# Kernel tuning notes

Measured on AMD Instinct MI355X. Metric: run time of the kernel, lower is better.

## Reference

```python
import jax, jax.numpy as jnp
import numpy as np
import math

B, T = 32, 64
VOCAB = 50005
EMB = 512
HID = 1024
SES = 1024
KNOW = 8785
NEG = math.exp(-100)

def _glorot(key, shape):
    fan_in, fan_out = shape[1], shape[0]
    lim = (6.0 / (fan_in + fan_out)) ** 0.5
    return jax.random.uniform(key, shape, jnp.float32, -lim, lim)

def setup_inputs() -> dict:
    key = jax.random.key(0)
    ks = jax.random.split(key, 16)
    inp = {}
    inp['ses_encoding'] = jax.random.normal(ks[0], (B, 1, SES), jnp.float32)
    inp['know_encoding'] = jax.random.normal(ks[1], (B, 1, SES), jnp.float32)
    inp['target'] = jax.random.randint(ks[2], (B, T), 0, 50000)
    inp['embed_w'] = jax.random.normal(ks[3], (VOCAB, EMB), jnp.float32) * 0.02
    # GRU params (PyTorch layout: W_ih [3H, E], W_hh [3H, H], gate order r,z,n)
    s = 1.0 / (HID ** 0.5)
    inp['W_ih'] = jax.random.uniform(ks[4], (3 * HID, EMB), jnp.float32, -s, s)
    inp['W_hh'] = jax.random.uniform(ks[5], (3 * HID, HID), jnp.float32, -s, s)
    inp['b_ih'] = jax.random.uniform(ks[6], (3 * HID,), jnp.float32, -s, s)
    inp['b_hh'] = jax.random.uniform(ks[7], (3 * HID,), jnp.float32, -s, s)
    inp['ses_to_dec_w'] = _glorot(ks[8], (HID, SES))
    inp['ses_to_dec_b'] = jnp.zeros((HID,), jnp.float32)
    inp['dec_inf_w'] = _glorot(ks[9], (2 * EMB, HID))
    inp['ses_inf_w'] = _glorot(ks[10], (2 * EMB, SES))
    inp['emb_inf_w'] = _glorot(ks[11], (2 * EMB, EMB))
    inp['emb_inf_b'] = jnp.zeros((2 * EMB,), jnp.float32)
    inp['W1'] = jax.random.normal(ks[12], (VOCAB, SES), jnp.float32) * 0.02
    inp['W2'] = jax.random.normal(ks[13], (VOCAB, SES), jnp.float32) * 0.02
    inp['W3'] = jax.random.normal(ks[14], (VOCAB, 2 * EMB), jnp.float32) * 0.02
    inp['W4'] = jax.random.normal(ks[15], (VOCAB, EMB), jnp.float32) * 0.02
    inp['know_vote_w'] = _glorot(jax.random.fold_in(key, 99), (KNOW, SES))
    return inp

def _gru_step(x, h, W_ih, W_hh, b_ih, b_hh):
    # x: [B,E], h: [B,H]
    gi = x @ W_ih.T + b_ih
    gh = h @ W_hh.T + b_hh
    ir, iz, inn = jnp.split(gi, 3, axis=-1)
    hr, hz, hn = jnp.split(gh, 3, axis=-1)
    r = jax.nn.sigmoid(ir + hr)
    z = jax.nn.sigmoid(iz + hz)
    n = jnp.tanh(inn + r * hn)
    return (1.0 - z) * h + z * n  # torch: h' = (1-z)*n + z*h with torch z; note torch formula

def _gru_step_torch(x, h, W_ih, W_hh, b_ih, b_hh):
    gi = x @ W_ih.T + b_ih
    gh = h @ W_hh.T + b_hh
    ir, iz, inn = jnp.split(gi, 3, axis=-1)
    hr, hz, hn = jnp.split(gh, 3, axis=-1)
    r = jax.nn.sigmoid(ir + hr)
    z = jax.nn.sigmoid(iz + hz)
    n = jnp.tanh(inn + r * hn)
    return (1.0 - z) * n + z * h

def reference(ses_encoding, know_encoding, target, embed_w, W_ih, W_hh, b_ih, b_hh,
              ses_to_dec_w, ses_to_dec_b, dec_inf_w, ses_inf_w, emb_inf_w, emb_inf_b,
              W1, W2, W3, W4, know_vote_w):
    ses = ses_encoding[:, 0, :]    # [B, SES]
    know = know_encoding[:, 0, :]  # [B, SES]
    target_emb = embed_w[target]   # [B, T, E]

    h0 = jnp.tanh(ses @ ses_to_dec_w.T + ses_to_dec_b)  # [B, H]

    # time-invariant pieces
    ses_inf_vec = ses @ ses_inf_w.T                      # [B, 2E]
    l1 = ses @ W1.T                                      # [B, V]
    l2 = know @ W2.T                                     # [B, V]
    # knowledge mixture log-probs (constant over time)
    ks = know @ know_vote_w.T                            # [B, KNOW]
    ks = ks[:, :-1]                                      # drop last -> [B, KNOW-1]
    pad_l = jnp.full((ks.shape[0], 10), NEG, ks.dtype)
    pad_r = jnp.full((ks.shape[0], VOCAB - 10 - (KNOW - 1)), NEG, ks.dtype)
    know_scores = jnp.concatenate([pad_l, ks, pad_r], axis=1)  # [B, V]
    know_probs = jax.nn.log_softmax(know_scores, axis=-1)      # [B, V]
    gate_const = l1 + l2                                 # [B, V]

    def step(h, emb_t):
        # emb_t: [B, E]
        h_new = _gru_step_torch(emb_t, h, W_ih, W_hh, b_ih, b_hh)  # [B, H]
        dec_hid_vec = h_new @ dec_inf_w.T                          # [B, 2E]
        target_inf = emb_t @ emb_inf_w.T + emb_inf_b               # [B, 2E]
        total = dec_hid_vec + ses_inf_vec + target_inf             # [B, 2E]
        mx = jnp.max(total.reshape(total.shape[0], EMB, 2), axis=-1)  # maxout -> [B, E]
        logits = mx @ embed_w.T                                    # shared embedding -> [B, V]
        hid_probs = jax.nn.log_softmax(logits, axis=-1)
        l3 = h_new @ W3.T                                          # note: W3 applied to hid_o [B,H]... but W3 is [V,2E]
        l4 = emb_t @ W4.T                                          # [B, V]
        gate = jax.nn.sigmoid(gate_const + l3 + l4)                # [B, V]
        final = gate * hid_probs + (1.0 - gate) * know_probs       # [B, V]
        return h_new, final

    # target_emb time-major for scan
    _, outs = jax.lax.scan(step, h0, jnp.swapaxes(target_emb, 0, 1))
    final_scores_all = jnp.swapaxes(outs, 0, 1)  # [B, T, V]
    return final_scores_all
```

## Files before the change

### kernel.cpp

```cpp
#include <hip/hip_runtime.h>

constexpr int VOC  = 50005;
constexpr int VOCP = 50048;
constexpr int VOCP2= 50176;
constexpr int NTM  = 391;
constexpr int NTMP = 400;
constexpr int KSN  = 8784;
constexpr int KSNP = 8832;
constexpr float NPAD = 41221.0f;

typedef unsigned short u16;
typedef __attribute__((ext_vector_type(4))) float f32x4;
typedef __attribute__((ext_vector_type(8))) short bf16x8;

__device__ __forceinline__ float dot4(float4 a, float4 b) {
    return a.x*b.x + a.y*b.y + a.z*b.z + a.w*b.w;
}
__device__ __forceinline__ float sigmoidf_(float x) { return 1.0f / (1.0f + expf(-x)); }
__device__ __forceinline__ u16 f2bf(float f) {
    unsigned x = __float_as_uint(f);
    return (u16)((x + 0x7FFFu + ((x >> 16) & 1u)) >> 16);
}
__device__ __forceinline__ float bf2f(u16 u) { return __uint_as_float(((unsigned)u) << 16); }
template<int AUX>
__device__ __forceinline__ void gload_lds16x(const void* g, void* l) {
    __builtin_amdgcn_global_load_lds((const __attribute__((address_space(1))) unsigned int*)g,
                                     (__attribute__((address_space(3))) unsigned int*)l, 16, 0, AUX);
}
__device__ __forceinline__ void gload_lds16(const void* g, void* l) { gload_lds16x<0>(g, l); }
__device__ __forceinline__ void store_u16_sc(u16* p, u16 v) {
    asm volatile("global_store_short %0, %1, off sc0 sc1" :: "v"(p), "v"((unsigned)v) : "memory");
}

__global__ __launch_bounds__(256) void k_cvt(const float* __restrict__ src, u16* __restrict__ dst,
                                             int ncols, int sld, int dld) {
    int row = blockIdx.x;
    int c = (blockIdx.y * 256 + threadIdx.x) * 4;
    if (c >= ncols) return;
    float4 v = *(const float4*)(src + (size_t)row * sld + c);
    unsigned lo = f2bf(v.x) | ((unsigned)f2bf(v.y) << 16);
    unsigned hi = f2bf(v.z) | ((unsigned)f2bf(v.w) << 16);
    *(uint2*)(dst + (size_t)row * dld + c) = make_uint2(lo, hi);
}

__global__ __launch_bounds__(256) void k_pad0(u16* __restrict__ Aemb, u16* __restrict__ A34,
                                              u16* __restrict__ Awk) {
    int r = VOC + blockIdx.x;
    unsigned* p3 = (unsigned*)(A34 + (size_t)r * 1536);
    for (int i = threadIdx.x; i < 768; i += 256) p3[i] = 0;
    if (r < VOCP) {
        unsigned* pe = (unsigned*)(Aemb + (size_t)r * 512);
        if (threadIdx.x < 256) pe[threadIdx.x] = 0;
        unsigned* pw = (unsigned*)(Awk + (size_t)r * 2048);
        for (int i = threadIdx.x; i < 1024; i += 256) pw[i] = 0;
    }
}
__global__ __launch_bounds__(256) void k_padK(u16* __restrict__ kvwb) {
    int r = KSN + blockIdx.x;
    unsigned* p = (unsigned*)(kvwb + (size_t)r * 1024);
    for (int i = threadIdx.x; i < 512; i += 256) p[i] = 0;
}

__global__ __launch_bounds__(256) void k_bsk(const float* __restrict__ ses,
                                             const float* __restrict__ know,
                                             u16* __restrict__ Bsk) {
    int row = blockIdx.x;
    for (int c0 = threadIdx.x * 4; c0 < 2048; c0 += 1024) {
        uint2 val = make_uint2(0, 0);
        if (row < 32) {
            const float* srcp = (c0 < 1024) ? ses + (size_t)row * 1024 + c0
                                            : know + (size_t)row * 1024 + (c0 - 1024);
            float4 v = *(const float4*)srcp;
            val = make_uint2(f2bf(v.x) | ((unsigned)f2bf(v.y) << 16),
                             f2bf(v.z) | ((unsigned)f2bf(v.w) << 16));
        }
        *(uint2*)(Bsk + (size_t)row * 2048 + c0) = val;
    }
}

__global__ __launch_bounds__(128) void k_gather(const float* __restrict__ embed,
                                                const int* __restrict__ target,
                                                u16* __restrict__ BG) {
    int n = blockIdx.x;
    int row = target[n];
    int c = threadIdx.x * 4;
    float4 v = *(const float4*)(embed + (size_t)row * 512 + c);
    unsigned lo = f2bf(v.x) | ((unsigned)f2bf(v.y) << 16);
    unsigned hi = f2bf(v.z) | ((unsigned)f2bf(v.w) << 16);
    *(uint2*)(BG + (size_t)n * 1536 + 1024 + c) = make_uint2(lo, hi);
}

__global__ __launch_bounds__(256) void k_h0_sesinf(const float* __restrict__ ses,
                                                   const float* __restrict__ sdw,
                                                   const float* __restrict__ sdb,
                                                   const float* __restrict__ siw,
                                                   float* __restrict__ h0,
                                                   float* __restrict__ sesinf) {
    int g = blockIdx.x * 256 + threadIdx.x;
    int b = g & 31;
    int jg = g >> 5;
    int j0 = jg * 4;
    const float4* s4 = (const float4*)(ses + (size_t)b * 1024);
    const float4* wa[4];
    const float4* wc[4];
#pragma unroll
    for (int r = 0; r < 4; ++r) {
        wa[r] = (const float4*)(sdw + (size_t)(j0 + r) * 1024);
        wc[r] = (const float4*)(siw + (size_t)(j0 + r) * 1024);
    }
    float a[4] = {0, 0, 0, 0}, c[4] = {0, 0, 0, 0};
    for (int kq = 0; kq < 256; ++kq) {
        float4 sv = s4[kq];
#pragma unroll
        for (int r = 0; r < 4; ++r) { a[r] += dot4(sv, wa[r][kq]); c[r] += dot4(sv, wc[r][kq]); }
    }
#pragma unroll
    for (int r = 0; r < 4; ++r) {
        h0[b * 1024 + j0 + r] = tanhf(a[r] + sdb[j0 + r]);
        sesinf[b * 1024 + j0 + r] = c[r];
    }
}

__global__ __launch_bounds__(256) void k_lseknow(const float* __restrict__ ks,
                                                 float* __restrict__ lsek) {
    int b = blockIdx.x;
    int t = threadIdx.x;
    __shared__ float sm[256];
    float m = -1e30f;
    for (int j = t; j < KSN; j += 256) m = fmaxf(m, ks[(size_t)b * KSN + j]);
    sm[t] = m;
    __syncthreads();
    for (int s = 128; s > 0; s >>= 1) { if (t < s) sm[t] = fmaxf(sm[t], sm[t + s]); __syncthreads(); }
    m = fmaxf(sm[0], 0.0f);
    __syncthreads();
    float s = 0.0f;
    for (int j = t; j < KSN; j += 256) s += expf(ks[(size_t)b * KSN + j] - m);
    sm[t] = s;
    __syncthreads();
    for (int r = 128; r > 0; r >>= 1) { if (t < r) sm[t] += sm[t + r]; __syncthreads(); }
    if (t == 0) lsek[b] = m + logf(sm[0] + NPAD * expf(0.0f - m));
}

template<int EPI>
__global__ __launch_bounds__(256) void gemm_bt(
    const u16* __restrict__ A, int lda,
    const u16* __restrict__ B, int ldb, int K,
    const float* __restrict__ p0, const float* __restrict__ p1,
    float* __restrict__ q0, u16* __restrict__ q1,
    unsigned char* __restrict__ q2, float* __restrict__ q3)
{
    __shared__ u16 Asm[128 * 64];
    __shared__ u16 Bsm[128 * 64];
    const int tid = threadIdx.x;
    const int lane = tid & 63;
    const int w = tid >> 6;
    const int wm = w >> 1, wn = w & 1;
    const int nt = blockIdx.x, mt = blockIdx.y;

    f32x4 acc[4][4];
#pragma unroll
    for (int i = 0; i < 4; ++i)
#pragma unroll
        for (int j = 0; j < 4; ++j) acc[i][j] = (f32x4){0.f, 0.f, 0.f, 0.f};

    for (int kt = 0; kt < K; kt += 64) {
#pragma unroll
        for (int p = 0; p < 4; ++p) {
            int flat = (w * 4 + p) * 64 + lane;
            int row = flat >> 3, slot = flat & 7;
            int ss = slot ^ (row & 7);
            gload_lds16(A + (size_t)(mt * 128 + row) * lda + kt + ss * 8, Asm + flat * 8);
            gload_lds16(B + (size_t)(nt * 128 + row) * ldb + kt + ss * 8, Bsm + flat * 8);
        }
        __syncthreads();
#pragma unroll
        for (int kc = 0; kc < 2; ++kc) {
            bf16x8 af[4], bfr[4];
#pragma unroll
            for (int mi = 0; mi < 4; ++mi) {
                int row = wm * 64 + mi * 16 + (lane & 15);
                int bcol = kc * 64 + ((lane >> 4) << 4);
                af[mi] = *(const bf16x8*)((const char*)Asm + row * 128 + (bcol ^ ((row & 7) << 4)));
            }
#pragma unroll
            for (int ni = 0; ni < 4; ++ni) {
                int row = wn * 64 + ni * 16 + (lane & 15);
                int bcol = kc * 64 + ((lane >> 4) << 4);
                bfr[ni] = *(const bf16x8*)((const char*)Bsm + row * 128 + (bcol ^ ((row & 7) << 4)));
            }
#pragma unroll
            for (int mi = 0; mi < 4; ++mi)
#pragma unroll
                for (int ni = 0; ni < 4; ++ni)
                    acc[mi][ni] = __builtin_amdgcn_mfma_f32_16x16x32_bf16(af[mi], bfr[ni], acc[mi][ni], 0, 0, 0);
        }
        __syncthreads();
    }

    const int cl = lane & 15;
    const int rg = (lane >> 4) << 2;

    if constexpr (EPI == 0) {
#pragma unroll
        for (int mi = 0; mi < 4; ++mi) {
            int m0 = mt * 128 + wm * 64 + mi * 16 + rg;
            float4 bias = *(const float4*)(p0 + m0);
#pragma unroll
            for (int ni = 0; ni < 4; ++ni) {
                int n = nt * 128 + wn * 64 + ni * 16 + cl;
                float4 v;
                v.x = acc[mi][ni][0] + bias.x; v.y = acc[mi][ni][1] + bias.y;
                v.z = acc[mi][ni][2] + bias.z; v.w = acc[mi][ni][3] + bias.w;
                *(float4*)(q0 + (size_t)n * 3072 + m0) = v;
            }
        }
    }
    if constexpr (EPI == 1) {
#pragma unroll
        for (int mi = 0; mi < 4; ++mi) {
            int m0 = mt * 128 + wm * 64 + mi * 16 + rg;
            float4 eb4 = *(const float4*)(p1 + m0);
#pragma unroll
            for (int ni = 0; ni < 4; ++ni) {
                int n = nt * 128 + wn * 64 + ni * 16 + cl;
                int b = n >> 6;
                float v0 = acc[mi][ni][0] + p0[b * 1024 + m0 + 0] + eb4.x;
                float v1 = acc[mi][ni][1] + p0[b * 1024 + m0 + 1] + eb4.y;
                float v2 = acc[mi][ni][2] + p0[b * 1024 + m0 + 2] + eb4.z;
                float v3 = acc[mi][ni][3] + p0[b * 1024 + m0 + 3] + eb4.w;
                unsigned pk = f2bf(fmaxf(v0, v1)) | ((unsigned)f2bf(fmaxf(v2, v3)) << 16);
                *(unsigned*)(q1 + (size_t)n * 512 + (m0 >> 1)) = pk;
            }
        }
    }
    if constexpr (EPI == 3) {
        __shared__ float redm[2][128];
        __shared__ float reds[2][128];
#pragma unroll
        for (int mi = 0; mi < 4; ++mi) {
            int v0 = mt * 128 + wm * 64 + mi * 16 + rg;
#pragma unroll
            for (int ni = 0; ni < 4; ++ni) {
                int n = nt * 128 + wn * 64 + ni * 16 + cl;
                unsigned lo = f2bf(acc[mi][ni][0]) | ((unsigned)f2bf(acc[mi][ni][1]) << 16);
                unsigned hi = f2bf(acc[mi][ni][2]) | ((unsigned)f2bf(acc[mi][ni][3]) << 16);
                *(uint2*)(q1 + (size_t)n * VOCP + v0) = make_uint2(lo, hi);
            }
        }
#pragma unroll
        for (int ni = 0; ni < 4; ++ni) {
            float lm = -1e30f;
#pragma unroll
            for (int mi = 0; mi < 4; ++mi) {
                int v0 = mt * 128 + wm * 64 + mi * 16 + rg;
#pragma unroll
                for (int r = 0; r < 4; ++r)
                    if (v0 + r < VOC) lm = fmaxf(lm, acc[mi][ni][r]);
            }
            lm = fmaxf(lm, __shfl_xor(lm, 16));
            lm = fmaxf(lm, __shfl_xor(lm, 32));
            float s = 0.0f;
#pragma unroll
            for (int mi = 0; mi < 4; ++mi) {
                int v0 = mt * 128 + wm * 64 + mi * 16 + rg;
#pragma unroll
                for (int r = 0; r < 4; ++r)
                    if (v0 + r < VOC) s += expf(acc[mi][ni][r] - lm);
            }
            s += __shfl_xor(s, 16);
            s += __shfl_xor(s, 32);
            if (lane < 16) {
                redm[wm][wn * 64 + ni * 16 + lane] = lm;
                reds[wm][wn * 64 + ni * 16 + lane] = s;
            }
        }
        __syncthreads();
        if (tid < 128) {
            float m0_ = redm[0][tid], m1_ = redm[1][tid];
            float m = fmaxf(m0_, m1_);
            float s = reds[0][tid] * expf(m0_ - m) + reds[1][tid] * expf(m1_ - m);
            int n = nt * 128 + tid;
            q0[(size_t)n * NTMP + mt] = m;
            q3[(size_t)n * NTMP + mt] = s;
        }
    }
    if constexpr (EPI == 4) {
#pragma unroll
        for (int mi = 0; mi < 4; ++mi) {
            int m0 = mt * 128 + wm * 64 + mi * 16 + rg;
#pragma unroll
            for (int ni = 0; ni < 4; ++ni) {
                int n = nt * 128 + wn * 64 + ni * 16 + cl;
                if (n < 32) {
                    float4 v;
                    v.x = acc[mi][ni][0]; v.y = acc[mi][ni][1];
                    v.z = acc[mi][ni][2]; v.w = acc[mi][ni][3];
                    *(float4*)(q0 + (size_t)n * VOCP2 + m0) = v;
                }
            }
        }
    }
    if constexpr (EPI == 5) {
#pragma unroll
        for (int mi = 0; mi < 4; ++mi) {
            int m0 = mt * 128 + wm * 64 + mi * 16 + rg;
#pragma unroll
            for (int ni = 0; ni < 4; ++ni) {
                int n = nt * 128 + wn * 64 + ni * 16 + cl;
                if (n < 32 && m0 < KSN) {
                    float4 v;
                    v.x = acc[mi][ni][0]; v.y = acc[mi][ni][1];
                    v.z = acc[mi][ni][2]; v.w = acc[mi][ni][3];
                    *(float4*)(q0 + (size_t)n * KSN + m0) = v;
                }
            }
        }
    }
}

__global__ __launch_bounds__(512, 2) void gemm_gate8(
    const u16* __restrict__ A,
    const u16* __restrict__ B,
    const float* __restrict__ gc2,
    unsigned char* __restrict__ g8)
{
    constexpr int K = 1536, NT = K / 32;
    __shared__ __align__(16) char smem[98304];
    const int tid = threadIdx.x;
    const int lane = tid & 63;
    const int w = tid >> 6;
    const int wm = w >> 2;
    const int wn = w & 3;
    const int lrow = lane & 15;
    const int g = lane >> 4;

    int bid = blockIdx.x;
    int wg = (bid & 7) * 196 + (bid >> 3);
    int mt = wg >> 3;
    int nt = wg & 7;
    const size_t arow0 = (size_t)mt * 256;
    const size_t brow0 = (size_t)nt * 256;

#define SWZ(r) (((r) & 3) ^ (((r) >> 2) & 3))
    auto stageA = [&](int t) {
        char* dst = smem + (t % 3) * 16384;
        int kt = t * 32;
#pragma unroll
        for (int q = 0; q < 2; ++q) {
            int flat = q * 512 + tid;
            int row = flat >> 2, s = flat & 3;
            int ss = s ^ SWZ(row);
            gload_lds16(A + (arow0 + row) * 1536 + kt + ss * 8, dst + flat * 16);
        }
    };
    auto stageB = [&](int t) {
        char* dst = smem + 49152 + (t % 3) * 16384;
        int kt = t * 32;
#pragma unroll
        for (int q = 0; q < 2; ++q) {
            int flat = q * 512 + tid;
            int row = flat >> 2, s = flat & 3;
            int ss = s ^ SWZ(row);
            gload_lds16(B + (brow0 + row) * 1536 + kt + ss * 8, dst + flat * 16);
        }
    };

    f32x4 acc[8][4];
#pragma unroll
    for (int i = 0; i < 8; ++i)
#pragma unroll
        for (int j = 0; j < 4; ++j) acc[i][j] = (f32x4){0.f, 0.f, 0.f, 0.f};

    stageA(0); stageB(0); stageA(1); stageB(1);
    asm volatile("s_waitcnt vmcnt(4)" ::: "memory");
    __builtin_amdgcn_sched_barrier(0);
    __builtin_amdgcn_s_barrier();

    auto tile_body = [&](int t, bool prefetch) {
        char* Ab = smem + (t % 3) * 16384;
        char* Bb = smem + 49152 + (t % 3) * 16384;
        if (prefetch) stageA(t + 2);
        bf16x8 bf[4], af[4];
#pragma unroll
        for (int ni = 0; ni < 4; ++ni) {
            int r = wn * 64 + ni * 16 + lrow;
            bf[ni] = *(const bf16x8*)(Bb + r * 64 + (g ^ SWZ(r)) * 16);
        }
#pragma unroll
        for (int mi = 0; mi < 4; ++mi) {
            int r = wm * 128 + mi * 16 + lrow;
            af[mi] = *(const bf16x8*)(Ab + r * 64 + (g ^ SWZ(r)) * 16);
        }
        __builtin_amdgcn_s_setprio(1);
#pragma unroll
        for (int mi = 0; mi < 4; ++mi)
#pragma unroll
            for (int ni = 0; ni < 4; ++ni)
                acc[mi][ni] = __builtin_amdgcn_mfma_f32_16x16x32_bf16(af[mi], bf[ni], acc[mi][ni], 0, 0, 0);
        __builtin_amdgcn_s_setprio(0);
        if (prefetch) stageB(t + 2);
#pragma unroll
        for (int mi = 0; mi < 4; ++mi) {
            int r = wm * 128 + 64 + mi * 16 + lrow;
            af[mi] = *(const bf16x8*)(Ab + r * 64 + (g ^ SWZ(r)) * 16);
        }
        __builtin_amdgcn_s_setprio(1);
#pragma unroll
        for (int mi = 0; mi < 4; ++mi)
#pragma unroll
            for (int ni = 0; ni < 4; ++ni)
                acc[4 + mi][ni] = __builtin_amdgcn_mfma_f32_16x16x32_bf16(af[mi], bf[ni], acc[4 + mi][ni], 0, 0, 0);
        __builtin_amdgcn_s_setprio(0);
    };

    for (int t = 0; t < NT - 2; ++t) {
        tile_body(t, true);
        asm volatile("s_waitcnt vmcnt(4)" ::: "memory");
        __builtin_amdgcn_sched_barrier(0);
        __builtin_amdgcn_s_barrier();
    }
    tile_body(NT - 2, false);
    asm volatile("s_waitcnt vmcnt(0)" ::: "memory");
    __builtin_amdgcn_sched_barrier(0);
    __builtin_amdgcn_s_barrier();
    tile_body(NT - 1, false);

    const int rg = g << 2;
    const int b = nt * 4 + wn;
    const float* gcrow = gc2 + (size_t)b * VOCP2;
#pragma unroll
    for (int a = 0; a < 8; ++a) {
        int v0 = mt * 256 + wm * 128 + (a >> 2) * 64 + (a & 3) * 16 + rg;
        float4 gcv = *(const float4*)(gcrow + v0);
#pragma unroll
        for (int ni = 0; ni < 4; ++ni) {
            int n = nt * 256 + wn * 64 + ni * 16 + lrow;
            unsigned pk = 0;
#pragma unroll
            for (int r = 0; r < 4; ++r) {
                float garg = acc[a][ni][r] + ((const float*)&gcv)[r];
                float gate = 1.0f / (1.0f + expf(-garg));
                pk |= ((unsigned)(int)(gate * 255.0f + 0.5f)) << (8 * r);
            }
            *(unsigned*)(g8 + (size_t)n * VOCP2 + v0) = pk;
        }
    }
#undef SWZ
}

__global__ __launch_bounds__(256, 1) void k_gru_m4(const u16* __restrict__ WhhB,
                                                   const float* __restrict__ GI,
                                                   const float* __restrict__ bhh,
                                                   const u16* __restrict__ h0b,
                                                   u16* __restrict__ BG,
                                                   unsigned* __restrict__ flags) {
    __shared__ __align__(16) char smem[131072];
    const int tid = threadIdx.x;
    const int lane = tid & 63;
    const int w = tid >> 6;
    const int jb = blockIdx.x;
    const int j0 = jb * 16;
    const int jl = tid & 15, bp = tid >> 4;
    const int je = j0 + jl;
    const float bh0 = bhh[je], bh1 = bhh[1024 + je], bh2 = bhh[2048 + je];
    char* Bbase = smem + 98304 + w * 8192;

#pragma unroll
    for (int it = 0; it < 24; ++it) {
        int flat = (it * 4 + w) * 64 + lane;
        int r = flat >> 7, s = flat & 127;
        int ss = s ^ (r & 7);
        int gr = (r >> 4) * 1024 + j0 + (r & 15);
        gload_lds16(WhhB + (size_t)gr * 1024 + ss * 8, smem + (size_t)flat * 16);
    }

    float hpv[2];
#pragma unroll
    for (int rb = 0; rb < 2; ++rb)
        hpv[rb] = bf2f(h0b[(size_t)(bp * 2 + rb) * 1024 + je]);

    const int lrow = lane & 15;
    const int ksel = lane >> 4;

    for (int t = 0; t < 64; ++t) {
        const u16* hsrc = (t == 0) ? h0b : BG + (size_t)(t - 1) * 1536;
        const size_t hstr = (t == 0) ? 1024 : (size_t)64 * 1536;

        float gi0[2], gi1[2], gi2[2];
#pragma unroll
        for (int rb = 0; rb < 2; ++rb) {
            const float* gp = GI + ((size_t)((bp * 2 + rb) * 64 + t)) * 3072 + je;
            gi0[rb] = gp[0]; gi1[rb] = gp[1024]; gi2[rb] = gp[2048];
        }
        __builtin_amdgcn_sched_barrier(0);

        auto stageB = [&](int c) {
            char* dst = Bbase + (c & 1) * 4096;
            int kq0 = w * 256 + c * 64;
#pragma unroll
            for (int q = 0; q < 4; ++q) {
                int flat = q * 64 + lane;
                int r = flat >> 3, s = flat & 7;
                int ss = s ^ (r & 7);
                gload_lds16x<0x11>(hsrc + (size_t)r * hstr + kq0 + ss * 8,
                                   dst + (size_t)flat * 16);
            }
        };
        stageB(0); stageB(1);
        if (t == 0) {
            __syncthreads();
        } else {
            asm volatile("s_waitcnt vmcnt(4)" ::: "memory");
        }
        __builtin_amdgcn_sched_barrier(0);

        f32x4 acc[3][2];
#pragma unroll
        for (int mi = 0; mi < 3; ++mi)
#pragma unroll
            for (int ni = 0; ni < 2; ++ni) acc[mi][ni] = (f32x4){0.f, 0.f, 0.f, 0.f};

#pragma unroll
        for (int c = 0; c < 4; ++c) {
            char* Bb = Bbase + (c & 1) * 4096;
#pragma unroll
            for (int ks = 0; ks < 2; ++ks) {
                int kb = ks * 64 + ksel * 16;
                bf16x8 bfr[2];
#pragma unroll
                for (int ni = 0; ni < 2; ++ni) {
                    int br = ni * 16 + lrow;
                    bfr[ni] = *(const bf16x8*)(Bb + br * 128 + (kb ^ ((br & 7) << 4)));
                }
                int kA = w * 512 + c * 128 + kb;
#pragma unroll
                for (int mi = 0; mi < 3; ++mi) {
                    int ar = mi * 16 + lrow;
                    bf16x8 af = *(const bf16x8*)(smem + ar * 2048 + (kA ^ ((ar & 7) << 4)));
#pragma unroll
                    for (int ni = 0; ni < 2; ++ni)
                        acc[mi][ni] = __builtin_amdgcn_mfma_f32_16x16x32_bf16(af, bfr[ni], acc[mi][ni], 0, 0, 0);
                }
            }
            asm volatile("s_waitcnt lgkmcnt(0)" ::: "memory");
            __builtin_amdgcn_sched_barrier(0);
            if (c < 2) {
                stageB(c + 2);
                asm volatile("s_waitcnt vmcnt(4)" ::: "memory");
            } else if (c == 2) {
                asm volatile("s_waitcnt vmcnt(0)" ::: "memory");
            }
            __builtin_amdgcn_sched_barrier(0);
        }

        float (*epiw)[33] = (float(*)[33])Bbase;
        {
            const int rg = (lane >> 4) << 2;
#pragma unroll
            for (int mi = 0; mi < 3; ++mi)
#pragma unroll
                for (int ni = 0; ni < 2; ++ni) {
                    int m0 = mi * 16 + rg;
                    int cb = ni * 16 + lrow;
#pragma unroll
                    for (int r = 0; r < 4; ++r) epiw[m0 + r][cb] = acc[mi][ni][r];
                }
        }
        asm volatile("s_waitcnt lgkmcnt(0)" ::: "memory");
        __builtin_amdgcn_s_barrier();

#pragma unroll
        for (int rb = 0; rb < 2; ++rb) {
            int b = bp * 2 + rb;
            float s0 = 0.f, s1 = 0.f, s2 = 0.f;
#pragma unroll
            for (int ww = 0; ww < 4; ++ww) {
                float (*ep)[33] = (float(*)[33])(smem + 98304 + ww * 8192);
                s0 += ep[jl][b]; s1 += ep[16 + jl][b]; s2 += ep[32 + jl][b];
            }
            float rr = sigmoidf_(gi0[rb] + s0 + bh0);
            float zz = sigmoidf_(gi1[rb] + s1 + bh1);
            float nn = tanhf(gi2[rb] + rr * (s2 + bh2));
            float hnew = (1.0f - zz) * nn + zz * hpv[rb];
            hpv[rb] = hnew;
            store_u16_sc(BG + ((size_t)(b * 64 + t)) * 1536 + je, f2bf(hnew));
        }

        if (t < 63) {
            asm volatile("s_waitcnt vmcnt(0)" ::: "memory");
            __syncthreads();
            if (tid == 0)
                __hip_atomic_store(&flags[jb], (unsigned)(t + 1),
                                   __ATOMIC_RELAXED, __HIP_MEMORY_SCOPE_AGENT);
            unsigned tgt = (unsigned)(t + 1);
            while (true) {
                unsigned v = __hip_atomic_load(&flags[lane],
                                               __ATOMIC_RELAXED, __HIP_MEMORY_SCOPE_AGENT);
                if (__all(v >= tgt)) break;
                __builtin_amdgcn_s_sleep(1);
            }
            __builtin_amdgcn_sched_barrier(0);
        }
    }
}

__global__ __launch_bounds__(256) void k_lse(const float* __restrict__ pmax,
                                             const float* __restrict__ psum,
                                             float* __restrict__ lse) {
    int n = blockIdx.x;
    int t = threadIdx.x;
    __shared__ float sm[256];
    const float* pm = pmax + (size_t)n * NTMP;
    const float* ps = psum + (size_t)n * NTMP;
    float m = -1e30f;
    for (int p = t; p < NTM; p += 256) m = fmaxf(m, pm[p]);
    sm[t] = m;
    __syncthreads();
    for (int s = 128; s > 0; s >>= 1) { if (t < s) sm[t] = fmaxf(sm[t], sm[t + s]); __syncthreads(); }
    m = sm[0];
    __syncthreads();
    float s = 0.0f;
    for (int p = t; p < NTM; p += 256) s += ps[p] * expf(pm[p] - m);
    sm[t] = s;
    __syncthreads();
    for (int r = 128; r > 0; r >>= 1) { if (t < r) sm[t] += sm[t + r]; __syncthreads(); }
    if (t == 0) lse[n] = m + logf(sm[0]);
}

__global__ __launch_bounds__(256) void k_final(const u16* __restrict__ Lb,
                                               const unsigned char* __restrict__ g8,
                                               const float* __restrict__ lse,
                                               const float* __restrict__ ks,
                                               const float* __restrict__ lsek,
                                               float* __restrict__ out) {
    int n = blockIdx.y;
    int b = n >> 6;
    float lsen = lse[n], lkb = lsek[b];
    int base = blockIdx.x * 2048;
#pragma unroll
    for (int i = 0; i < 8; ++i) {
        int v = base + i * 256 + threadIdx.x;
        if (v < VOC) {
            float L = bf2f(Lb[(size_t)n * VOCP + v]);
            float g = g8[(size_t)n * VOCP2 + v] * (1.0f / 255.0f);
            float kp = ((v >= 10 && v < 10 + KSN) ? ks[(size_t)b * KSN + (v - 10)] : 0.0f) - lkb;
            out[(size_t)n * VOC + v] = g * (L - lsen) + (1.0f - g) * kp;
        }
    }
}

extern "C" void kernel_launch(void* const* d_in, const int* in_sizes, int n_in,
                              void* d_out, int out_size, void* d_ws, size_t ws_size,
                              hipStream_t stream) {
    const float* ses    = (const float*)d_in[0];
    const float* know   = (const float*)d_in[1];
    const int*   target = (const int*)d_in[2];
    const float* embed  = (const float*)d_in[3];
    const float* Wih    = (const float*)d_in[4];
    const float* Whh    = (const float*)d_in[5];
    const float* bih    = (const float*)d_in[6];
    const float* bhh    = (const float*)d_in[7];
    const float* sdw    = (const float*)d_in[8];
    const float* sdb    = (const float*)d_in[9];
    const float* dw     = (const float*)d_in[10];
    const float* siw    = (const float*)d_in[11];
    const float* ew     = (const float*)d_in[12];
    const float* eb     = (const float*)d_in[13];
    const float* W1     = (const float*)d_in[14];
    const float* W2     = (const float*)d_in[15];
    const float* W3     = (const float*)d_in[16];
    const float* W4     = (const float*)d_in[17];
    const float* kvw    = (const float*)d_in[18];

    char* ws = (char*)d_ws;
    size_t o = 0;
    auto alloc = [&](size_t bytes) { char* r = ws + o; o += (bytes + 255) & ~(size_t)255; return r; };
    u16*   Aemb  = (u16*)  alloc((size_t)VOCP * 512 * 2);
    u16*   A34   = (u16*)  alloc((size_t)VOCP2 * 1536 * 2);
    u16*   Adwew = (u16*)  alloc((size_t)1024 * 1536 * 2);
    u16*   Wihb  = (u16*)  alloc((size_t)3072 * 512 * 2);
    u16*   WhhB  = (u16*)  alloc((size_t)3072 * 1024 * 2);
    u16*   h0b   = (u16*)  alloc((size_t)32 * 1024 * 2);
    u16*   BG    = (u16*)  alloc((size_t)2048 * 1536 * 2);
    u16*   BL    = (u16*)  alloc((size_t)2048 * 512 * 2);
    float* GI    = (float*)alloc((size_t)2048 * 3072 * 4);
    float* h0    = (float*)alloc((size_t)32 * 1024 * 4);
    float* sesinf= (float*)alloc((size_t)32 * 1024 * 4);
    float* gc    = (float*)alloc((size_t)32 * VOCP2 * 4);
    float* ksb   = (float*)alloc((size_t)32 * KSN * 4);
    float* lsek  = (float*)alloc(256);
    float* lse   = (float*)alloc((size_t)2048 * 4);
    unsigned* flags = (unsigned*)alloc(256);
    float* pmax  = (float*)alloc((size_t)2048 * NTMP * 4);
    float* psum  = (float*)alloc((size_t)2048 * NTMP * 4);
    unsigned char* g8 = (unsigned char*)alloc((size_t)2048 * VOCP2);
    u16*   Lb    = (u16*)  alloc((size_t)2048 * VOCP * 2);
    u16*   Bsk   = (u16*)  alloc((size_t)128 * 2048 * 2);
    float* out = (float*)d_out;

    u16*   kvwb  = (u16*)g8;
    u16*   Awk   = Lb;

    hipMemsetAsync(flags, 0, 256, stream);

    k_cvt<<<dim3(VOC, 1), 256, 0, stream>>>(embed, Aemb, 512, 512, 512);
    k_cvt<<<dim3(VOC, 1), 256, 0, stream>>>(W3, A34, 1024, 1024, 1536);
    k_cvt<<<dim3(VOC, 1), 256, 0, stream>>>(W4, A34 + 1024, 512, 512, 1536);
    k_cvt<<<dim3(VOC, 1), 256, 0, stream>>>(W1, Awk, 1024, 1024, 2048);
    k_cvt<<<dim3(VOC, 1), 256, 0, stream>>>(W2, Awk + 1024, 1024, 1024, 2048);
    k_cvt<<<dim3(KSN, 1), 256, 0, stream>>>(kvw, kvwb, 1024, 1024, 1024);
    k_pad0<<<dim3(VOCP2 - VOC), 256, 0, stream>>>(Aemb, A34, Awk);
    k_padK<<<dim3(KSNP - KSN), 256, 0, stream>>>(kvwb);
    k_cvt<<<dim3(1024, 1), 256, 0, stream>>>(dw, Adwew, 1024, 1024, 1536);
    k_cvt<<<dim3(1024, 1), 256, 0, stream>>>(ew, Adwew + 1024, 512, 512, 1536);
    k_cvt<<<dim3(3072, 1), 256, 0, stream>>>(Wih, Wihb, 512, 512, 512);
    k_cvt<<<dim3(3072, 1), 256, 0, stream>>>(Whh, WhhB, 1024, 1024, 1024);
    k_bsk<<<dim3(128), 256, 0, stream>>>(ses, know, Bsk);

    k_gather<<<dim3(2048), 128, 0, stream>>>(embed, target, BG);
    k_h0_sesinf<<<dim3(32), 256, 0, stream>>>(ses, sdw, sdb, siw, h0, sesinf);
    k_cvt<<<dim3(32, 1), 256, 0, stream>>>(h0, h0b, 1024, 1024, 1024);

    gemm_bt<4><<<dim3(1, NTM), 256, 0, stream>>>(Awk, 2048, Bsk, 2048, 2048,
                                                 nullptr, nullptr, gc, nullptr, nullptr, nullptr);
    gemm_bt<5><<<dim3(1, 69), 256, 0, stream>>>(kvwb, 1024, Bsk + 1024, 2048, 1024,
                                                nullptr, nullptr, ksb, nullptr, nullptr, nullptr);
    k_lseknow<<<dim3(32), 256, 0, stream>>>(ksb, lsek);

    gemm_bt<0><<<dim3(16, 24), 256, 0, stream>>>(Wihb, 512, BG + 1024, 1536, 512,
                                                 bih, nullptr, GI, nullptr, nullptr, nullptr);
    k_gru_m4<<<dim3(64), 256, 0, stream>>>(WhhB, GI, bhh, h0b, BG, flags);
    gemm_bt<1><<<dim3(16, 8), 256, 0, stream>>>(Adwew, 1536, BG, 1536, 1536,
                                                sesinf, eb, nullptr, BL, nullptr, nullptr);
    gemm_gate8<<<dim3(1568), 512, 0, stream>>>(A34, BG, gc, g8);
    gemm_bt<3><<<dim3(16, NTM), 256, 0, stream>>>(Aemb, 512, BL, 512, 512,
                                                  nullptr, nullptr, pmax, Lb, nullptr, psum);
    k_lse<<<dim3(2048), 256, 0, stream>>>(pmax, psum, lse);
    k_final<<<dim3(25, 2048), 256, 0, stream>>>(Lb, g8, lse, ksb, lsek, out);
}
```

Before: 1.665 ms.

## Restructure gate GEMM into 8-phase ping-pong pipeline with K=64 tiles

Rewrites the main loop of the bf16 gate GEMM to use 64-wide K tiles in a double-buffered 128KB LDS layout with an XOR swizzle over 8 chunks. Each K tile is split into four phases, and each phase interleaves one global-to-LDS prefetch with a slice of MFMAs, separated by barriers. B fragments are loaded once per tile and reused across phases. The aim is finer overlap of loads and matrix math and fewer LDS reads per MFMA, at the cost of occupancy dropping from two blocks per CU to one and more barriers.

```diff
diff --git a/kernel.cpp b/kernel.cpp
--- a/kernel.cpp
+++ b/kernel.cpp
@@ -318,14 +318,13 @@
     }
 }
 
-__global__ __launch_bounds__(512, 2) void gemm_gate8(
+__global__ __launch_bounds__(512, 1) void gemm_gate8(
     const u16* __restrict__ A,
     const u16* __restrict__ B,
     const float* __restrict__ gc2,
     unsigned char* __restrict__ g8)
 {
-    constexpr int K = 1536, NT = K / 32;
-    __shared__ __align__(16) char smem[98304];
+    __shared__ __align__(16) char smem[131072];
     const int tid = threadIdx.x;
     const int lane = tid & 63;
     const int w = tid >> 6;
@@ -341,27 +340,26 @@
     const size_t arow0 = (size_t)mt * 256;
     const size_t brow0 = (size_t)nt * 256;
 
-#define SWZ(r) (((r) & 3) ^ (((r) >> 2) & 3))
-    auto stageA = [&](int t) {
-        char* dst = smem + (t % 3) * 16384;
-        int kt = t * 32;
+    auto stageA = [&](int T, int h) {
+        char* dst = smem + (T & 1) * 65536 + h * 16384;
+        const u16* src = A + (arow0 + h * 128) * 1536 + T * 64;
 #pragma unroll
         for (int q = 0; q < 2; ++q) {
             int flat = q * 512 + tid;
-            int row = flat >> 2, s = flat & 3;
-            int ss = s ^ SWZ(row);
-            gload_lds16(A + (arow0 + row) * 1536 + kt + ss * 8, dst + flat * 16);
+            int r = flat >> 3, s = flat & 7;
+            int ss = s ^ (r & 7);
+            gload_lds16(src + (size_t)r * 1536 + ss * 8, dst + flat * 16);
         }
     };
-    auto stageB = [&](int t) {
-        char* dst = smem + 49152 + (t % 3) * 16384;
-        int kt = t * 32;
+    auto stageB = [&](int T, int h) {
+        char* dst = smem + (T & 1) * 65536 + 32768 + h * 16384;
+        const u16* src = B + (brow0 + h * 128) * 1536 + T * 64;
 #pragma unroll
         for (int q = 0; q < 2; ++q) {
             int flat = q * 512 + tid;
-            int row = flat >> 2, s = flat & 3;
-            int ss = s ^ SWZ(row);
-            gload_lds16(B + (brow0 + row) * 1536 + kt + ss * 8, dst + flat * 16);
+            int r = flat >> 3, s = flat & 7;
+            int ss = s ^ (r & 7);
+            gload_lds16(src + (size_t)r * 1536 + ss * 8, dst + flat * 16);
         }
     };
 
@@ -371,66 +369,81 @@
 #pragma unroll
         for (int j = 0; j < 4; ++j) acc[i][j] = (f32x4){0.f, 0.f, 0.f, 0.f};
 
-    stageA(0); stageB(0); stageA(1); stageB(1);
-    asm volatile("s_waitcnt vmcnt(4)" ::: "memory");
-    __builtin_amdgcn_sched_barrier(0);
+    bf16x8 bf[4][2];
+    auto loadB_ = [&](int d) {
+        char* Bb = smem + d * 65536 + 32768 + (wn >> 1) * 16384;
+#pragma unroll
+        for (int ni = 0; ni < 4; ++ni) {
+            int r = (wn & 1) * 64 + ni * 16 + lrow;
+#pragma unroll
+            for (int kk = 0; kk < 2; ++kk)
+                bf[ni][kk] = *(const bf16x8*)(Bb + r * 128 + ((kk * 64 + g * 16) ^ ((r & 7) << 4)));
+        }
+    };
+
+#define GPH(D, Q, LB, STG, VM)                                                        \
+    {                                                                                 \
+        if (LB) loadB_(D);                                                            \
+        bf16x8 af[2][2];                                                              \
+        char* Ab = smem + (D) * 65536 + wm * 16384;                                   \
+        _Pragma("unroll") for (int mi = 0; mi < 2; ++mi) {                            \
+            int r = ((Q) * 2 + mi) * 16 + lrow;                                       \
+            _Pragma("unroll") for (int kk = 0; kk < 2; ++kk)                          \
+                af[mi][kk] = *(const bf16x8*)(Ab + r * 128 +                          \
+                                ((kk * 64 + g * 16) ^ ((r & 7) << 4)));               \
+        }                                                                             \
+        STG;                                                                          \
+        __builtin_amdgcn_s_barrier();                                                 \
+        asm volatile("s_waitcnt lgkmcnt(0)" ::: "memory");                            \
+        __builtin_amdgcn_sched_barrier(0);                                            \
+        __builtin_amdgcn_s_setprio(1);                                                \
+        _Pragma("unroll") for (int kk = 0; kk < 2; ++kk)                              \
+            _Pragma("unroll") for (int mi = 0; mi < 2; ++mi)                          \
+                _Pragma("unroll") for (int ni = 0; ni < 4; ++ni)                      \
+                    acc[(Q) * 2 + mi][ni] = __builtin_amdgcn_mfma_f32_16x16x32_bf16(  \
+                        af[mi][kk], bf[ni][kk], acc[(Q) * 2 + mi][ni], 0, 0, 0);      \
+        __builtin_amdgcn_s_setprio(0);                                                \
+        VM;                                                                           \
+        __builtin_amdgcn_s_barrier();                                                 \
+    }
+#define VM4 asm volatile("s_waitcnt vmcnt(4)" ::: "memory"); __builtin_amdgcn_sched_barrier(0)
+#define VM0 asm volatile("s_waitcnt vmcnt(0)" ::: "memory"); __builtin_amdgcn_sched_barrier(0)
+#define NOP (void)0
+
+    stageB(0, 0); stageB(0, 1); stageA(0, 0); stageA(0, 1); stageB(1, 0); stageB(1, 1);
+    VM4;
     __builtin_amdgcn_s_barrier();
 
-    auto tile_body = [&](int t, bool prefetch) {
-        char* Ab = smem + (t % 3) * 16384;
-        char* Bb = smem + 49152 + (t % 3) * 16384;
-        if (prefetch) stageA(t + 2);
-        bf16x8 bf[4], af[4];
-#pragma unroll
-        for (int ni = 0; ni < 4; ++ni) {
-            int r = wn * 64 + ni * 16 + lrow;
-            bf[ni] = *(const bf16x8*)(Bb + r * 64 + (g ^ SWZ(r)) * 16);
-        }
-#pragma unroll
-        for (int mi = 0; mi < 4; ++mi) {
-            int r = wm * 128 + mi * 16 + lrow;
-            af[mi] = *(const bf16x8*)(Ab + r * 64 + (g ^ SWZ(r)) * 16);
-        }
-        __builtin_amdgcn_s_setprio(1);
-#pragma unroll
-        for (int mi = 0; mi < 4; ++mi)
-#pragma unroll
-            for (int ni = 0; ni < 4; ++ni)
-                acc[mi][ni] = __builtin_amdgcn_mfma_f32_16x16x32_bf16(af[mi], bf[ni], acc[mi][ni], 0, 0, 0);
-        __builtin_amdgcn_s_setprio(0);
-        if (prefetch) stageB(t + 2);
-#pragma unroll
-        for (int mi = 0; mi < 4; ++mi) {
-            int r = wm * 128 + 64 + mi * 16 + lrow;
-            af[mi] = *(const bf16x8*)(Ab + r * 64 + (g ^ SWZ(r)) * 16);
-        }
-        __builtin_amdgcn_s_setprio(1);
-#pragma unroll
-        for (int mi = 0; mi < 4; ++mi)
-#pragma unroll
-            for (int ni = 0; ni < 4; ++ni)
-                acc[4 + mi][ni] = __builtin_amdgcn_mfma_f32_16x16x32_bf16(af[mi], bf[ni], acc[4 + mi][ni], 0, 0, 0);
-        __builtin_amdgcn_s_setprio(0);
-    };
-
-    for (int t = 0; t < NT - 2; ++t) {
-        tile_body(t, true);
-        asm volatile("s_waitcnt vmcnt(4)" ::: "memory");
-        __builtin_amdgcn_sched_barrier(0);
-        __builtin_amdgcn_s_barrier();
-    }
-    tile_body(NT - 2, false);
-    asm volatile("s_waitcnt vmcnt(0)" ::: "memory");
-    __builtin_amdgcn_sched_barrier(0);
-    __builtin_amdgcn_s_barrier();
-    tile_body(NT - 1, false);
+    for (int i = 0; i < 11; ++i) {
+        int T0 = 2 * i, T1 = 2 * i + 1;
+        GPH(0, 0, true,  stageA(T1, 0),     NOP);
+        GPH(0, 1, false, stageA(T1, 1),     NOP);
+        GPH(0, 2, false, stageB(T0 + 2, 0), NOP);
+        GPH(0, 3, false, stageB(T0 + 2, 1), VM4);
+        GPH(1, 0, true,  stageA(T0 + 2, 0), NOP);
+        GPH(1, 1, false, stageA(T0 + 2, 1), NOP);
+        GPH(1, 2, false, stageB(T1 + 2, 0), NOP);
+        GPH(1, 3, false, stageB(T1 + 2, 1), VM4);
+    }
+    GPH(0, 0, true,  stageA(23, 0), NOP);
+    GPH(0, 1, false, stageA(23, 1), NOP);
+    GPH(0, 2, false, NOP,           NOP);
+    GPH(0, 3, false, NOP,           VM0);
+    GPH(1, 0, true,  NOP,           NOP);
+    GPH(1, 1, false, NOP,           NOP);
+    GPH(1, 2, false, NOP,           NOP);
+    GPH(1, 3, false, NOP,           NOP);
+#undef GPH
+#undef VM4
+#undef VM0
+#undef NOP
 
     const int rg = g << 2;
     const int b = nt * 4 + wn;
     const float* gcrow = gc2 + (size_t)b * VOCP2;
 #pragma unroll
-    for (int a = 0; a < 8; ++a) {
-        int v0 = mt * 256 + wm * 128 + (a >> 2) * 64 + (a & 3) * 16 + rg;
+    for (int m = 0; m < 8; ++m) {
+        int v0 = mt * 256 + wm * 128 + m * 16 + rg;
         float4 gcv = *(const float4*)(gcrow + v0);
 #pragma unroll
         for (int ni = 0; ni < 4; ++ni) {
@@ -438,14 +451,13 @@
             unsigned pk = 0;
 #pragma unroll
             for (int r = 0; r < 4; ++r) {
-                float garg = acc[a][ni][r] + ((const float*)&gcv)[r];
+                float garg = acc[m][ni][r] + ((const float*)&gcv)[r];
                 float gate = 1.0f / (1.0f + expf(-garg));
                 pk |= ((unsigned)(int)(gate * 255.0f + 0.5f)) << (8 * r);
             }
             *(unsigned*)(g8 + (size_t)n * VOCP2 + v0) = pk;
         }
     }
-#undef SWZ
 }
 
 __global__ __launch_bounds__(256, 1) void k_gru_m4(const u16* __restrict__ WhhB,
```

Measured after the change: 1.634 ms. No clear change (-1.9%).
